# Performance work log

Measured on AMD Instinct MI355X. Metric: run time of the kernel, lower is better.

Reference implementation:

```python
import jax, jax.numpy as jnp
import numpy as np

B, T, D = 2, 2048, 2048
H, KV, HD = 32, 8, 64
N_REP = H // KV
THETA = 10000.0
NEG_INF = -1e30


def _rope_tables(seq_len, head_dim, theta):
    inv_freq = 1.0 / (theta ** (jnp.arange(0, head_dim, 2, dtype=jnp.float32) / head_dim))
    t = jnp.arange(seq_len, dtype=jnp.float32)
    freqs = jnp.outer(t, inv_freq)                 # (T, HD/2)
    emb = jnp.concatenate([freqs, freqs], axis=-1)  # (T, HD)
    return jnp.cos(emb), jnp.sin(emb)


def _rotate_half(x):
    half = x.shape[-1] // 2
    return jnp.concatenate([-x[..., half:], x[..., :half]], axis=-1)


def setup_inputs() -> dict:
    key = jax.random.key(0)
    ks = jax.random.split(key, 5)
    s = 0.02  # keep logits in a sane range
    x = jax.random.normal(ks[0], (B, T, D), dtype=jnp.float32)
    Wq = jax.random.normal(ks[1], (D, H * HD), dtype=jnp.float32) * s
    Wk = jax.random.normal(ks[2], (D, KV * HD), dtype=jnp.float32) * s
    Wv = jax.random.normal(ks[3], (D, KV * HD), dtype=jnp.float32) * s
    Wo = jax.random.normal(ks[4], (D, D), dtype=jnp.float32) * s
    cos, sin = _rope_tables(T, HD, THETA)  # start_pos=0 since past_kv is None
    return {"x": x, "Wq": Wq, "Wk": Wk, "Wv": Wv, "Wo": Wo, "cos": cos, "sin": sin}


def reference(x, Wq, Wk, Wv, Wo, cos, sin):
    b, t, _ = x.shape
    # projections -> (B, heads, T, HD)
    q = (x @ Wq).reshape(b, t, H, HD).transpose(0, 2, 1, 3)
    k = (x @ Wk).reshape(b, t, KV, HD).transpose(0, 2, 1, 3)
    v = (x @ Wv).reshape(b, t, KV, HD).transpose(0, 2, 1, 3)
    # RoPE (cos/sin broadcast over batch and heads)
    c = cos[None, None, :, :]
    s = sin[None, None, :, :]
    q = q * c + _rotate_half(q) * s
    k = k * c + _rotate_half(k) * s
    # GQA: broadcast KV heads instead of repeat_interleave.
    # repeat_interleave(n_rep, dim=1) maps query head h -> kv head h // n_rep,
    # which equals reshape H -> (KV, N_REP).
    qg = q.reshape(b, KV, N_REP, t, HD)
    scale = 1.0 / jnp.sqrt(jnp.float32(HD))
    scores = jnp.einsum('bgrtd,bgsd->bgrts', qg, k) * scale  # (B,KV,N_REP,T,T)
    causal = jnp.tril(jnp.ones((t, t), dtype=bool))
    scores = jnp.where(causal[None, None, None, :, :], scores, NEG_INF)
    probs = jax.nn.softmax(scores, axis=-1)
    y = jnp.einsum('bgrts,bgsd->bgrtd', probs, v)            # (B,KV,N_REP,T,HD)
    y = y.reshape(b, H, t, HD).transpose(0, 2, 1, 3).reshape(b, t, H * HD)
    return y @ Wo
```

## Files before the change

### kernel.cpp

```cpp
#include <hip/hip_runtime.h>
#include <hip/hip_bf16.h>

constexpr int Bc  = 2;
constexpr int Tc  = 2048;
constexpr int Dc  = 2048;
constexpr int Hc  = 32;
constexpr int KVc = 8;
constexpr int HDc = 64;
constexpr int Mrows = Bc * Tc;
constexpr int QKVW  = 3072;
constexpr float SCALE = 0.125f;

typedef __attribute__((ext_vector_type(8))) short  bf16x8;
typedef __attribute__((ext_vector_type(4))) short  short4v;
typedef __attribute__((ext_vector_type(4))) float  f32x4;

__device__ __forceinline__ short f2bf(float f) {
    unsigned u = __builtin_bit_cast(unsigned, f);
    unsigned r = (u + 0x7FFFu + ((u >> 16) & 1u)) >> 16;
    return (short)(unsigned short)r;
}

__device__ __forceinline__ void load_lds16(const void* g, void* l) {
    __builtin_amdgcn_global_load_lds(
        (const __attribute__((address_space(1))) unsigned int*)g,
        (__attribute__((address_space(3))) unsigned int*)l,
        16, 0, 0);
}

__global__ void conv_bf16(const float* __restrict__ in, short* __restrict__ out, int n) {
    int i = (blockIdx.x * blockDim.x + threadIdx.x) * 8;
    if (i >= n) return;
    f32x4 a = *(const f32x4*)(in + i);
    f32x4 b = *(const f32x4*)(in + i + 4);
    bf16x8 o;
    o[0] = f2bf(a[0]); o[1] = f2bf(a[1]); o[2] = f2bf(a[2]); o[3] = f2bf(a[3]);
    o[4] = f2bf(b[0]); o[5] = f2bf(b[1]); o[6] = f2bf(b[2]); o[7] = f2bf(b[3]);
    *(bf16x8*)(out + i) = o;
}

__global__ __launch_bounds__(256) void transpose_conv(const float* __restrict__ in,
                                                      short* __restrict__ out,
                                                      int N, int ldo, int n0r) {
    __shared__ float T[64][68];
    const int k0 = blockIdx.y * 64;
    const int n0 = blockIdx.x * 64;
    const int t  = threadIdx.x;
    const int c4 = (t & 15) * 4;
    const int rr = t >> 4;
#pragma unroll
    for (int r = 0; r < 4; ++r) {
        int k = rr + 16 * r;
        float4 v = *(const float4*)(in + (size_t)(k0 + k) * N + n0 + c4);
        *(float4*)&T[k][c4] = v;
    }
    __syncthreads();
#pragma unroll
    for (int r = 0; r < 4; ++r) {
        int n = rr + 16 * r;
        short4v s;
        s[0] = f2bf(T[c4 + 0][n]); s[1] = f2bf(T[c4 + 1][n]);
        s[2] = f2bf(T[c4 + 2][n]); s[3] = f2bf(T[c4 + 3][n]);
        *(short4v*)(out + (size_t)(n0r + n0 + n) * ldo + k0 + c4) = s;
    }
}

__global__ __launch_bounds__(256) void gemm_mfma(const short* __restrict__ A,
                                                 const short* __restrict__ Bt,
                                                 float* __restrict__ C,
                                                 int M, int N, int K) {
    __shared__ short Al[128 * 64];
    __shared__ short Bl[128 * 64];
    const int tid = threadIdx.x;
    const int l  = tid & 63;
    const int w  = tid >> 6;
    const int lr = l & 15;
    const int lg = l >> 4;
    const int wm = w >> 1, wn = w & 1;
    const int bm = blockIdx.y * 128;
    const int bn = blockIdx.x * 128;

    f32x4 acc[4][4];
#pragma unroll
    for (int i = 0; i < 4; ++i)
#pragma unroll
        for (int j = 0; j < 4; ++j) acc[i][j] = f32x4{0.f, 0.f, 0.f, 0.f};

    const int srow_off = l >> 3;
    const int sunit    = l & 7;

    for (int k0 = 0; k0 < K; k0 += 64) {
        __syncthreads();
#pragma unroll
        for (int j = 0; j < 4; ++j) {
            const int q   = w + 4 * j;
            const int row = 8 * q + srow_off;
            const int ug  = sunit ^ (row & 7);
            load_lds16(A  + (size_t)(bm + row) * K + k0 + ug * 8, (short*)Al + 512 * q);
            load_lds16(Bt + (size_t)(bn + row) * K + k0 + ug * 8, (short*)Bl + 512 * q);
        }
        __syncthreads();

#pragma unroll
        for (int ks = 0; ks < 2; ++ks) {
            bf16x8 af[4], bf[4];
#pragma unroll
            for (int mb = 0; mb < 4; ++mb) {
                const int row = wm * 64 + mb * 16 + lr;
                const int u   = (ks * 4 + lg) ^ (row & 7);
                af[mb] = *(const bf16x8*)(Al + row * 64 + u * 8);
            }
#pragma unroll
            for (int nb = 0; nb < 4; ++nb) {
                const int row = wn * 64 + nb * 16 + lr;
                const int u   = (ks * 4 + lg) ^ (row & 7);
                bf[nb] = *(const bf16x8*)(Bl + row * 64 + u * 8);
            }
#pragma unroll
            for (int mb = 0; mb < 4; ++mb)
#pragma unroll
                for (int nb = 0; nb < 4; ++nb)
                    acc[mb][nb] = __builtin_amdgcn_mfma_f32_16x16x32_bf16(
                        af[mb], bf[nb], acc[mb][nb], 0, 0, 0);
        }
    }

#pragma unroll
    for (int mb = 0; mb < 4; ++mb)
#pragma unroll
        for (int r = 0; r < 4; ++r) {
            const int row = bm + wm * 64 + mb * 16 + lg * 4 + r;
            float* cp = C + (size_t)row * N + bn + wn * 64 + lr;
#pragma unroll
            for (int nb = 0; nb < 4; ++nb) cp[nb * 16] = acc[mb][nb][r];
        }
}

__global__ void rope_fused(float* __restrict__ qkv,
                           const float* __restrict__ cosT,
                           const float* __restrict__ sinT, int total) {
    int idx = blockIdx.x * blockDim.x + threadIdx.x;
    if (idx >= total) return;
    int d   = idx & 31;
    int hh  = (idx >> 5) % 40;
    int row = idx / (32 * 40);
    int t   = row & (Tc - 1);
    int col = (hh < 32) ? hh * 64 : 2048 + (hh - 32) * 64;
    float c = cosT[t * HDc + d];
    float s = sinT[t * HDc + d];
    float* p = qkv + (size_t)row * QKVW + col;
    float x0 = p[d];
    float x1 = p[d + 32];
    p[d]      = x0 * c - x1 * s;
    p[d + 32] = x1 * c + x0 * s;
}

__global__ __launch_bounds__(256) void attn_mfma(const float* __restrict__ qkv,
                                                 short* __restrict__ yb) {
    __shared__ short Ks[64 * 64];
    __shared__ short Vt[64][72];
    __shared__ short Ps[4][16][72];

    const int tid = threadIdx.x;
    const int l   = tid & 63;
    const int w   = tid >> 6;
    const int lr  = l & 15;
    const int lg  = l >> 4;
    const int qt0 = blockIdx.x * 64;
    const int h   = blockIdx.y;
    const int b   = blockIdx.z;
    const int g   = h >> 2;
    const int qw0 = qt0 + w * 16;

    bf16x8 qf[2];
    {
        const float* qrow = qkv + (size_t)(b * Tc + qw0 + lr) * QKVW + h * 64;
#pragma unroll
        for (int s = 0; s < 2; ++s) {
            f32x4 a0 = *(const f32x4*)(qrow + s * 32 + lg * 8);
            f32x4 a1 = *(const f32x4*)(qrow + s * 32 + lg * 8 + 4);
            bf16x8 t;
            t[0] = f2bf(a0[0] * SCALE); t[1] = f2bf(a0[1] * SCALE);
            t[2] = f2bf(a0[2] * SCALE); t[3] = f2bf(a0[3] * SCALE);
            t[4] = f2bf(a1[0] * SCALE); t[5] = f2bf(a1[1] * SCALE);
            t[6] = f2bf(a1[2] * SCALE); t[7] = f2bf(a1[3] * SCALE);
            qf[s] = t;
        }
    }

    f32x4 o[4];
#pragma unroll
    for (int i = 0; i < 4; ++i) o[i] = f32x4{0.f, 0.f, 0.f, 0.f};
    float mr[4], ls[4];
#pragma unroll
    for (int i = 0; i < 4; ++i) { mr[i] = -1e30f; ls[i] = 0.f; }

    const float* kb_ = qkv + (size_t)(b * Tc) * QKVW + 2048 + g * 64;
    const float* vb_ = qkv + (size_t)(b * Tc) * QKVW + 2560 + g * 64;
    const int ntiles = qt0 / 64 + 1;

    const int kd0   = (tid & 15) * 4;
    const int kunit = kd0 >> 3;
    const int khalf = (kd0 & 4) << 1;
    const int vkey  = (tid & 31) * 2;
    const int vd0   = (tid >> 5) * 8;

    for (int t = 0; t < ntiles; ++t) {
        const int kv0 = t * 64;
#pragma unroll
        for (int r = 0; r < 4; ++r) {
            const int key = (tid >> 4) + 16 * r;
            f32x4 a = *(const f32x4*)(kb_ + (size_t)(kv0 + key) * QKVW + kd0);
            short4v s4;
            s4[0] = f2bf(a[0]); s4[1] = f2bf(a[1]);
            s4[2] = f2bf(a[2]); s4[3] = f2bf(a[3]);
            *(short4v*)((char*)Ks + key * 128 + ((kunit ^ (key & 7)) << 4) + khalf) = s4;
        }
        {
            const float* r0 = vb_ + (size_t)(kv0 + vkey) * QKVW + vd0;
            const float* r1 = r0 + QKVW;
            f32x4 a0 = *(const f32x4*)(r0);
            f32x4 a1 = *(const f32x4*)(r0 + 4);
            f32x4 b0 = *(const f32x4*)(r1);
            f32x4 b1 = *(const f32x4*)(r1 + 4);
#pragma unroll
            for (int j = 0; j < 4; ++j) {
                unsigned pk0 = (unsigned short)f2bf(a0[j]) |
                               ((unsigned)(unsigned short)f2bf(b0[j]) << 16);
                unsigned pk1 = (unsigned short)f2bf(a1[j]) |
                               ((unsigned)(unsigned short)f2bf(b1[j]) << 16);
                *(unsigned*)&Vt[vd0 + j][vkey]     = pk0;
                *(unsigned*)&Vt[vd0 + 4 + j][vkey] = pk1;
            }
        }
        __syncthreads();

        f32x4 c[4];
#pragma unroll
        for (int kbk = 0; kbk < 4; ++kbk) {
            const int key = lr + 16 * kbk;
            const char* kr = (const char*)Ks + key * 128;
            bf16x8 k0 = *(const bf16x8*)(kr + ((lg       ^ (key & 7)) << 4));
            bf16x8 k1 = *(const bf16x8*)(kr + (((4 + lg) ^ (key & 7)) << 4));
            f32x4 acc = f32x4{0.f, 0.f, 0.f, 0.f};
            acc = __builtin_amdgcn_mfma_f32_16x16x32_bf16(qf[0], k0, acc, 0, 0, 0);
            acc = __builtin_amdgcn_mfma_f32_16x16x32_bf16(qf[1], k1, acc, 0, 0, 0);
            c[kbk] = acc;
        }

        if (t == ntiles - 1) {
#pragma unroll
            for (int kbk = 0; kbk < 4; ++kbk)
#pragma unroll
                for (int r = 0; r < 4; ++r)
                    if (kv0 + lr + 16 * kbk > qw0 + lg * 4 + r) c[kbk][r] = -1e30f;
        }

#pragma unroll
        for (int r = 0; r < 4; ++r) {
            float tm = fmaxf(fmaxf(c[0][r], c[1][r]), fmaxf(c[2][r], c[3][r]));
            tm = fmaxf(tm, __shfl_xor(tm, 1));
            tm = fmaxf(tm, __shfl_xor(tm, 2));
            tm = fmaxf(tm, __shfl_xor(tm, 4));
            tm = fmaxf(tm, __shfl_xor(tm, 8));
            const float mnew = fmaxf(mr[r], tm);
            const float corr = __expf(mr[r] - mnew);
            mr[r] = mnew;
            float rs = 0.f;
#pragma unroll
            for (int kbk = 0; kbk < 4; ++kbk) {
                float p = __expf(c[kbk][r] - mnew);
                c[kbk][r] = p;
                rs += p;
            }
            rs += __shfl_xor(rs, 1);
            rs += __shfl_xor(rs, 2);
            rs += __shfl_xor(rs, 4);
            rs += __shfl_xor(rs, 8);
            ls[r] = ls[r] * corr + rs;
#pragma unroll
            for (int db = 0; db < 4; ++db) o[db][r] *= corr;
#pragma unroll
            for (int kbk = 0; kbk < 4; ++kbk)
                Ps[w][lg * 4 + r][lr + 16 * kbk] = f2bf(c[kbk][r]);
        }

#pragma unroll
        for (int ks = 0; ks < 2; ++ks) {
            bf16x8 pa = *(const bf16x8*)&Ps[w][lr][lg * 8 + ks * 32];
#pragma unroll
            for (int db = 0; db < 4; ++db) {
                bf16x8 vv = *(const bf16x8*)&Vt[lr + 16 * db][lg * 8 + ks * 32];
                o[db] = __builtin_amdgcn_mfma_f32_16x16x32_bf16(pa, vv, o[db], 0, 0, 0);
            }
        }
        __syncthreads();
    }

#pragma unroll
    for (int r = 0; r < 4; ++r) {
        const float inv = 1.0f / ls[r];
        short* yp = yb + (size_t)(b * Tc + qw0 + lg * 4 + r) * Dc + h * 64;
#pragma unroll
        for (int db = 0; db < 4; ++db)
            yp[lr + 16 * db] = f2bf(o[db][r] * inv);
    }
}

extern "C" void kernel_launch(void* const* d_in, const int* in_sizes, int n_in,
                              void* d_out, int out_size, void* d_ws, size_t ws_size,
                              hipStream_t stream) {
    const float* x    = (const float*)d_in[0];
    const float* Wq   = (const float*)d_in[1];
    const float* Wk   = (const float*)d_in[2];
    const float* Wv   = (const float*)d_in[3];
    const float* Wo   = (const float*)d_in[4];
    const float* cosT = (const float*)d_in[5];
    const float* sinT = (const float*)d_in[6];
    float* out = (float*)d_out;

    short* xb    = (short*)d_ws;
    short* Wqkvt = xb + (size_t)Mrows * Dc;
    short* Wot   = Wqkvt + (size_t)QKVW * Dc;
    short* ybuf  = Wot + (size_t)Dc * Dc;
    float* qkv   = (float*)(ybuf + (size_t)Mrows * Dc);

    conv_bf16<<<(Mrows * Dc / 8 + 255) / 256, 256, 0, stream>>>(x, xb, Mrows * Dc);
    transpose_conv<<<dim3(Dc / 64, Dc / 64), 256, 0, stream>>>(Wq, Wqkvt, Dc, Dc, 0);
    transpose_conv<<<dim3(512 / 64, Dc / 64), 256, 0, stream>>>(Wk, Wqkvt, 512, Dc, 2048);
    transpose_conv<<<dim3(512 / 64, Dc / 64), 256, 0, stream>>>(Wv, Wqkvt, 512, Dc, 2560);
    transpose_conv<<<dim3(Dc / 64, Dc / 64), 256, 0, stream>>>(Wo, Wot, Dc, Dc, 0);

    gemm_mfma<<<dim3(QKVW / 128, Mrows / 128), 256, 0, stream>>>(xb, Wqkvt, qkv, Mrows, QKVW, Dc);

    {
        int total = Mrows * (Hc + KVc) * 32;
        rope_fused<<<(total + 255) / 256, 256, 0, stream>>>(qkv, cosT, sinT, total);
    }

    attn_mfma<<<dim3(Tc / 64, Hc, Bc), 256, 0, stream>>>(qkv, ybuf);

    gemm_mfma<<<dim3(Dc / 128, Mrows / 128), 256, 0, stream>>>(ybuf, Wot, out, Mrows, Dc, Dc);
}
```

Measured before the change: 527.5 us.

## Pre-pack Q/K/V to bf16 head-major layouts and restructure attention kernel

RoPE now writes pre-scaled bf16 Q and bf16 K in head-major layouts, and a new kernel transposes V to bf16 V^T. The attention kernel becomes single-wave blocks of 16 query rows that read K and V directly from global memory with no LDS staging. Each block handles a pair of mirrored query tiles to balance causal work. The softmax rescale is skipped when the running max is unchanged, and the GEMM gets a block-index swizzle meant to improve L2 locality. Removing per-tile fp32->bf16 conversion and LDS sync is traded for more global/L2 traffic per wave and scratch buffers that reuse the xb/Wqkvt workspace.

```diff
diff --git a/kernel.cpp b/kernel.cpp
--- a/kernel.cpp
+++ b/kernel.cpp
@@ -77,8 +77,13 @@
     const int lr = l & 15;
     const int lg = l >> 4;
     const int wm = w >> 1, wn = w & 1;
-    const int bm = blockIdx.y * 128;
-    const int bn = blockIdx.x * 128;
+
+    const int nwg = gridDim.x * gridDim.y;
+    const int bid0 = blockIdx.y * gridDim.x + blockIdx.x;
+    const int cpx = nwg >> 3;
+    const int swz = (bid0 & 7) * cpx + (bid0 >> 3);
+    const int bm = (swz / gridDim.x) * 128;
+    const int bn = (swz % gridDim.x) * 128;
 
     f32x4 acc[4][4];
 #pragma unroll
@@ -136,174 +141,170 @@
         }
 }
 
-__global__ void rope_fused(float* __restrict__ qkv,
-                           const float* __restrict__ cosT,
-                           const float* __restrict__ sinT, int total) {
+__global__ void rope_pack_qk(const float* __restrict__ qkv,
+                             const float* __restrict__ cosT,
+                             const float* __restrict__ sinT,
+                             short* __restrict__ qb, short* __restrict__ kb,
+                             int total) {
     int idx = blockIdx.x * blockDim.x + threadIdx.x;
     if (idx >= total) return;
     int d   = idx & 31;
     int hh  = (idx >> 5) % 40;
     int row = idx / (32 * 40);
     int t   = row & (Tc - 1);
-    int col = (hh < 32) ? hh * 64 : 2048 + (hh - 32) * 64;
+    int b   = row >> 11;
     float c = cosT[t * HDc + d];
     float s = sinT[t * HDc + d];
-    float* p = qkv + (size_t)row * QKVW + col;
-    float x0 = p[d];
-    float x1 = p[d + 32];
-    p[d]      = x0 * c - x1 * s;
-    p[d + 32] = x1 * c + x0 * s;
-}
-
-__global__ __launch_bounds__(256) void attn_mfma(const float* __restrict__ qkv,
-                                                 short* __restrict__ yb) {
-    __shared__ short Ks[64 * 64];
-    __shared__ short Vt[64][72];
-    __shared__ short Ps[4][16][72];
-
-    const int tid = threadIdx.x;
-    const int l   = tid & 63;
-    const int w   = tid >> 6;
-    const int lr  = l & 15;
-    const int lg  = l >> 4;
-    const int qt0 = blockIdx.x * 64;
-    const int h   = blockIdx.y;
-    const int b   = blockIdx.z;
-    const int g   = h >> 2;
-    const int qw0 = qt0 + w * 16;
-
-    bf16x8 qf[2];
-    {
-        const float* qrow = qkv + (size_t)(b * Tc + qw0 + lr) * QKVW + h * 64;
-#pragma unroll
-        for (int s = 0; s < 2; ++s) {
-            f32x4 a0 = *(const f32x4*)(qrow + s * 32 + lg * 8);
-            f32x4 a1 = *(const f32x4*)(qrow + s * 32 + lg * 8 + 4);
-            bf16x8 t;
-            t[0] = f2bf(a0[0] * SCALE); t[1] = f2bf(a0[1] * SCALE);
-            t[2] = f2bf(a0[2] * SCALE); t[3] = f2bf(a0[3] * SCALE);
-            t[4] = f2bf(a1[0] * SCALE); t[5] = f2bf(a1[1] * SCALE);
-            t[6] = f2bf(a1[2] * SCALE); t[7] = f2bf(a1[3] * SCALE);
-            qf[s] = t;
-        }
-    }
-
-    f32x4 o[4];
-#pragma unroll
-    for (int i = 0; i < 4; ++i) o[i] = f32x4{0.f, 0.f, 0.f, 0.f};
-    float mr[4], ls[4];
-#pragma unroll
-    for (int i = 0; i < 4; ++i) { mr[i] = -1e30f; ls[i] = 0.f; }
-
-    const float* kb_ = qkv + (size_t)(b * Tc) * QKVW + 2048 + g * 64;
-    const float* vb_ = qkv + (size_t)(b * Tc) * QKVW + 2560 + g * 64;
-    const int ntiles = qt0 / 64 + 1;
-
-    const int kd0   = (tid & 15) * 4;
-    const int kunit = kd0 >> 3;
-    const int khalf = (kd0 & 4) << 1;
-    const int vkey  = (tid & 31) * 2;
-    const int vd0   = (tid >> 5) * 8;
-
-    for (int t = 0; t < ntiles; ++t) {
-        const int kv0 = t * 64;
+    if (hh < 32) {
+        const float* p = qkv + (size_t)row * QKVW + hh * 64;
+        float x0 = p[d], x1 = p[d + 32];
+        short* qp = qb + (((size_t)(b * Hc + hh) * Tc + t) * 64);
+        qp[d]      = f2bf((x0 * c - x1 * s) * SCALE);
+        qp[d + 32] = f2bf((x1 * c + x0 * s) * SCALE);
+    } else {
+        int g = hh - 32;
+        const float* p = qkv + (size_t)row * QKVW + 2048 + g * 64;
+        float x0 = p[d], x1 = p[d + 32];
+        short* kp = kb + (((size_t)(b * KVc + g) * Tc + t) * 64);
+        kp[d]      = f2bf(x0 * c - x1 * s);
+        kp[d + 32] = f2bf(x1 * c + x0 * s);
+    }
+}
+
+__global__ __launch_bounds__(256) void pack_vt(const float* __restrict__ qkv,
+                                               short* __restrict__ vtb) {
+    __shared__ float T[64][68];
+    const int t0 = blockIdx.x * 64;
+    const int g  = blockIdx.y;
+    const int b  = blockIdx.z;
+    const int tt = threadIdx.x;
+    const int c4 = (tt & 15) * 4;
+    const int rr = tt >> 4;
+    const float* src = qkv + 2560 + g * 64;
+#pragma unroll
+    for (int r = 0; r < 4; ++r) {
+        int t = rr + 16 * r;
+        float4 v = *(const float4*)(src + (size_t)(b * Tc + t0 + t) * QKVW + c4);
+        *(float4*)&T[t][c4] = v;
+    }
+    __syncthreads();
+    short* dst = vtb + ((size_t)(b * KVc + g) * 64) * Tc;
+#pragma unroll
+    for (int r = 0; r < 4; ++r) {
+        int d = rr + 16 * r;
+        short4v s;
+        s[0] = f2bf(T[c4 + 0][d]); s[1] = f2bf(T[c4 + 1][d]);
+        s[2] = f2bf(T[c4 + 2][d]); s[3] = f2bf(T[c4 + 3][d]);
+        *(short4v*)(dst + (size_t)d * Tc + t0 + c4) = s;
+    }
+}
+
+__global__ __launch_bounds__(64) void attn_gqa(const short* __restrict__ qb,
+                                               const short* __restrict__ kb,
+                                               const short* __restrict__ vtb,
+                                               short* __restrict__ yb) {
+    __shared__ short Ps[16][72];
+    const int l  = threadIdx.x;
+    const int lr = l & 15;
+    const int lg = l >> 4;
+    const int h  = blockIdx.y;
+    const int b  = blockIdx.z;
+    const int g  = h >> 2;
+
+    const short* qhb = qb  + ((size_t)(b * Hc  + h) * Tc) * 64;
+    const short* khb = kb  + ((size_t)(b * KVc + g) * Tc) * 64;
+    const short* vhb = vtb + ((size_t)(b * KVc + g) * 64) * Tc;
+
+#pragma unroll
+    for (int half = 0; half < 2; ++half) {
+        const int j   = half ? (127 - (int)blockIdx.x) : (int)blockIdx.x;
+        const int qt0 = j * 16;
+
+        bf16x8 qf0 = *(const bf16x8*)(qhb + (size_t)(qt0 + lr) * 64 + lg * 8);
+        bf16x8 qf1 = *(const bf16x8*)(qhb + (size_t)(qt0 + lr) * 64 + 32 + lg * 8);
+
+        f32x4 o[4];
+#pragma unroll
+        for (int i = 0; i < 4; ++i) o[i] = f32x4{0.f, 0.f, 0.f, 0.f};
+        float mr[4], ls[4];
+#pragma unroll
+        for (int i = 0; i < 4; ++i) { mr[i] = -1e30f; ls[i] = 0.f; }
+
+        const int nsteps = (qt0 >> 6) + 1;
+        for (int st = 0; st < nsteps; ++st) {
+            const int kv0 = st * 64;
+
+            f32x4 c[4];
+#pragma unroll
+            for (int kbk = 0; kbk < 4; ++kbk) {
+                const short* kr = khb + (size_t)(kv0 + 16 * kbk + lr) * 64;
+                bf16x8 k0 = *(const bf16x8*)(kr + lg * 8);
+                bf16x8 k1 = *(const bf16x8*)(kr + 32 + lg * 8);
+                f32x4 acc = f32x4{0.f, 0.f, 0.f, 0.f};
+                acc = __builtin_amdgcn_mfma_f32_16x16x32_bf16(qf0, k0, acc, 0, 0, 0);
+                acc = __builtin_amdgcn_mfma_f32_16x16x32_bf16(qf1, k1, acc, 0, 0, 0);
+                c[kbk] = acc;
+            }
+
+            if (st == nsteps - 1) {
+#pragma unroll
+                for (int kbk = 0; kbk < 4; ++kbk)
+#pragma unroll
+                    for (int r = 0; r < 4; ++r)
+                        if (kv0 + lr + 16 * kbk > qt0 + lg * 4 + r) c[kbk][r] = -1e30f;
+            }
+
+#pragma unroll
+            for (int r = 0; r < 4; ++r) {
+                float tm = fmaxf(fmaxf(c[0][r], c[1][r]), fmaxf(c[2][r], c[3][r]));
+                tm = fmaxf(tm, __shfl_xor(tm, 1));
+                tm = fmaxf(tm, __shfl_xor(tm, 2));
+                tm = fmaxf(tm, __shfl_xor(tm, 4));
+                tm = fmaxf(tm, __shfl_xor(tm, 8));
+                if (tm > mr[r]) {
+                    const float corr = __expf(mr[r] - tm);
+                    mr[r] = tm;
+                    ls[r] *= corr;
+#pragma unroll
+                    for (int db = 0; db < 4; ++db) o[db][r] *= corr;
+                }
+                float rs = 0.f;
+#pragma unroll
+                for (int kbk = 0; kbk < 4; ++kbk) {
+                    float p = __expf(c[kbk][r] - mr[r]);
+                    c[kbk][r] = p;
+                    rs += p;
+                }
+                rs += __shfl_xor(rs, 1);
+                rs += __shfl_xor(rs, 2);
+                rs += __shfl_xor(rs, 4);
+                rs += __shfl_xor(rs, 8);
+                ls[r] += rs;
+#pragma unroll
+                for (int kbk = 0; kbk < 4; ++kbk)
+                    Ps[lg * 4 + r][lr + 16 * kbk] = f2bf(c[kbk][r]);
+            }
+
+#pragma unroll
+            for (int ks = 0; ks < 2; ++ks) {
+                bf16x8 pa = *(const bf16x8*)&Ps[lr][lg * 8 + ks * 32];
+#pragma unroll
+                for (int db = 0; db < 4; ++db) {
+                    bf16x8 vv = *(const bf16x8*)(vhb + (size_t)(db * 16 + lr) * Tc
+                                                 + kv0 + ks * 32 + lg * 8);
+                    o[db] = __builtin_amdgcn_mfma_f32_16x16x32_bf16(pa, vv, o[db], 0, 0, 0);
+                }
+            }
+        }
+
 #pragma unroll
         for (int r = 0; r < 4; ++r) {
-            const int key = (tid >> 4) + 16 * r;
-            f32x4 a = *(const f32x4*)(kb_ + (size_t)(kv0 + key) * QKVW + kd0);
-            short4v s4;
-            s4[0] = f2bf(a[0]); s4[1] = f2bf(a[1]);
-            s4[2] = f2bf(a[2]); s4[3] = f2bf(a[3]);
-            *(short4v*)((char*)Ks + key * 128 + ((kunit ^ (key & 7)) << 4) + khalf) = s4;
-        }
-        {
-            const float* r0 = vb_ + (size_t)(kv0 + vkey) * QKVW + vd0;
-            const float* r1 = r0 + QKVW;
-            f32x4 a0 = *(const f32x4*)(r0);
-            f32x4 a1 = *(const f32x4*)(r0 + 4);
-            f32x4 b0 = *(const f32x4*)(r1);
-            f32x4 b1 = *(const f32x4*)(r1 + 4);
-#pragma unroll
-            for (int j = 0; j < 4; ++j) {
-                unsigned pk0 = (unsigned short)f2bf(a0[j]) |
-                               ((unsigned)(unsigned short)f2bf(b0[j]) << 16);
-                unsigned pk1 = (unsigned short)f2bf(a1[j]) |
-                               ((unsigned)(unsigned short)f2bf(b1[j]) << 16);
-                *(unsigned*)&Vt[vd0 + j][vkey]     = pk0;
-                *(unsigned*)&Vt[vd0 + 4 + j][vkey] = pk1;
-            }
-        }
-        __syncthreads();
-
-        f32x4 c[4];
-#pragma unroll
-        for (int kbk = 0; kbk < 4; ++kbk) {
-            const int key = lr + 16 * kbk;
-            const char* kr = (const char*)Ks + key * 128;
-            bf16x8 k0 = *(const bf16x8*)(kr + ((lg       ^ (key & 7)) << 4));
-            bf16x8 k1 = *(const bf16x8*)(kr + (((4 + lg) ^ (key & 7)) << 4));
-            f32x4 acc = f32x4{0.f, 0.f, 0.f, 0.f};
-            acc = __builtin_amdgcn_mfma_f32_16x16x32_bf16(qf[0], k0, acc, 0, 0, 0);
-            acc = __builtin_amdgcn_mfma_f32_16x16x32_bf16(qf[1], k1, acc, 0, 0, 0);
-            c[kbk] = acc;
-        }
-
-        if (t == ntiles - 1) {
-#pragma unroll
-            for (int kbk = 0; kbk < 4; ++kbk)
-#pragma unroll
-                for (int r = 0; r < 4; ++r)
-                    if (kv0 + lr + 16 * kbk > qw0 + lg * 4 + r) c[kbk][r] = -1e30f;
-        }
-
-#pragma unroll
-        for (int r = 0; r < 4; ++r) {
-            float tm = fmaxf(fmaxf(c[0][r], c[1][r]), fmaxf(c[2][r], c[3][r]));
-            tm = fmaxf(tm, __shfl_xor(tm, 1));
-            tm = fmaxf(tm, __shfl_xor(tm, 2));
-            tm = fmaxf(tm, __shfl_xor(tm, 4));
-            tm = fmaxf(tm, __shfl_xor(tm, 8));
-            const float mnew = fmaxf(mr[r], tm);
-            const float corr = __expf(mr[r] - mnew);
-            mr[r] = mnew;
-            float rs = 0.f;
-#pragma unroll
-            for (int kbk = 0; kbk < 4; ++kbk) {
-                float p = __expf(c[kbk][r] - mnew);
-                c[kbk][r] = p;
-                rs += p;
-            }
-            rs += __shfl_xor(rs, 1);
-            rs += __shfl_xor(rs, 2);
-            rs += __shfl_xor(rs, 4);
-            rs += __shfl_xor(rs, 8);
-            ls[r] = ls[r] * corr + rs;
-#pragma unroll
-            for (int db = 0; db < 4; ++db) o[db][r] *= corr;
-#pragma unroll
-            for (int kbk = 0; kbk < 4; ++kbk)
-                Ps[w][lg * 4 + r][lr + 16 * kbk] = f2bf(c[kbk][r]);
-        }
-
-#pragma unroll
-        for (int ks = 0; ks < 2; ++ks) {
-            bf16x8 pa = *(const bf16x8*)&Ps[w][lr][lg * 8 + ks * 32];
-#pragma unroll
-            for (int db = 0; db < 4; ++db) {
-                bf16x8 vv = *(const bf16x8*)&Vt[lr + 16 * db][lg * 8 + ks * 32];
-                o[db] = __builtin_amdgcn_mfma_f32_16x16x32_bf16(pa, vv, o[db], 0, 0, 0);
-            }
-        }
-        __syncthreads();
-    }
-
-#pragma unroll
-    for (int r = 0; r < 4; ++r) {
-        const float inv = 1.0f / ls[r];
-        short* yp = yb + (size_t)(b * Tc + qw0 + lg * 4 + r) * Dc + h * 64;
-#pragma unroll
-        for (int db = 0; db < 4; ++db)
-            yp[lr + 16 * db] = f2bf(o[db][r] * inv);
+            const float inv = 1.0f / ls[r];
+            short* yp = yb + (size_t)(b * Tc + qt0 + lg * 4 + r) * Dc + h * 64;
+#pragma unroll
+            for (int db = 0; db < 4; ++db)
+                yp[lr + 16 * db] = f2bf(o[db][r] * inv);
+        }
     }
 }
 
@@ -324,6 +325,9 @@
     short* Wot   = Wqkvt + (size_t)QKVW * Dc;
     short* ybuf  = Wot + (size_t)Dc * Dc;
     float* qkv   = (float*)(ybuf + (size_t)Mrows * Dc);
+    short* qbp = xb;
+    short* kbp = Wqkvt;
+    short* vtb = Wqkvt + (size_t)Bc * KVc * Tc * 64;
 
     conv_bf16<<<(Mrows * Dc / 8 + 255) / 256, 256, 0, stream>>>(x, xb, Mrows * Dc);
     transpose_conv<<<dim3(Dc / 64, Dc / 64), 256, 0, stream>>>(Wq, Wqkvt, Dc, Dc, 0);
@@ -335,10 +339,11 @@
 
     {
         int total = Mrows * (Hc + KVc) * 32;
-        rope_fused<<<(total + 255) / 256, 256, 0, stream>>>(qkv, cosT, sinT, total);
-    }
-
-    attn_mfma<<<dim3(Tc / 64, Hc, Bc), 256, 0, stream>>>(qkv, ybuf);
+        rope_pack_qk<<<(total + 255) / 256, 256, 0, stream>>>(qkv, cosT, sinT, qbp, kbp, total);
+        pack_vt<<<dim3(Tc / 64, KVc, Bc), 256, 0, stream>>>(qkv, vtb);
+    }
+
+    attn_gqa<<<dim3(64, Hc, Bc), 64, 0, stream>>>(qbp, kbp, vtb, ybuf);
 
     gemm_mfma<<<dim3(Dc / 128, Mrows / 128), 256, 0, stream>>>(ybuf, Wot, out, Mrows, Dc, Dc);
 }
```

New measurement: 525.3 us. No clear change (-0.4%).
